# Kernel tuning notes

Hardware: AMD Instinct MI355X
Metric: run time of the kernel (lower is better)

Reference implementation:

```python
import jax, jax.numpy as jnp
import numpy as np

DM = 768            # d_model
DI = 1536           # d_inner = expand * d_model
P = 64              # headdim
H = DI // P         # 24 heads
N = 64              # d_state (Mamba2Simple default)
K = 4               # d_conv
CONVD = DI + 2 * N  # 1664
D_IN_PROJ = 2 * DI + 2 * N + H  # 3224
BATCH = 2
NVAL = 1024
L = NVAL
EPS = 1e-5

# static tail_order / swap_order index (transpose the rows x cols token grid, reversed)
_rows = int(NVAL ** 0.5)
_t = np.arange(NVAL).reshape(_rows, -1).T
_t = NVAL - 1 - _t
TAIL = _t.reshape(-1)
SEQ = jnp.asarray(np.concatenate([np.arange(L - NVAL), TAIL + (L - NVAL)]))


def _make_params(key, prefix):
    ks = jax.random.split(key, 6)
    dt = jnp.exp(jax.random.uniform(ks[2], (H,), minval=np.log(1e-3), maxval=np.log(1e-1)))
    return {
        prefix + 'ln_w': jnp.ones(DM, jnp.float32),
        prefix + 'ln_b': jnp.zeros(DM, jnp.float32),
        prefix + 'in_w': jax.random.normal(ks[0], (D_IN_PROJ, DM), jnp.float32) * 0.02,
        prefix + 'conv_w': jax.random.normal(ks[1], (CONVD, K), jnp.float32) * 0.1,
        prefix + 'conv_b': jnp.zeros(CONVD, jnp.float32),
        prefix + 'dt_bias': jnp.log(jnp.expm1(dt)),  # inverse softplus of dt in [1e-3, 1e-1]
        prefix + 'A_log': jnp.log(jax.random.uniform(ks[3], (H,), minval=1.0, maxval=16.0)),
        prefix + 'D': jnp.ones(H, jnp.float32),
        prefix + 'norm_w': jnp.ones(DI, jnp.float32),
        prefix + 'out_w': jax.random.normal(ks[4], (DM, DI), jnp.float32) * 0.02,
    }


def setup_inputs() -> dict:
    key = jax.random.key(0)
    k1, k2, k3 = jax.random.split(key, 3)
    inp = {'x': jax.random.normal(k1, (BATCH, L, DM), dtype=jnp.float32)}
    inp.update(_make_params(k2, 'f_'))
    inp.update(_make_params(k3, 'b_'))
    return inp


def _layernorm(x, w, b):
    m = jnp.mean(x, -1, keepdims=True)
    v = jnp.mean((x - m) ** 2, -1, keepdims=True)
    return (x - m) * jax.lax.rsqrt(v + EPS) * w + b


def _mamba2(x, in_w, conv_w, conv_b, dt_bias, A_log, Dp, norm_w, out_w):
    Bsz, Lseq, _ = x.shape
    zxbcdt = x @ in_w.T                                   # [B,L,3224]
    z, xBC, dt = jnp.split(zxbcdt, [DI, DI + CONVD], axis=-1)
    dt = jax.nn.softplus(dt + dt_bias)                    # [B,L,H]
    # causal depthwise conv1d over channels
    xc = jnp.transpose(xBC, (0, 2, 1))                    # [B,C,L]
    xc = jax.lax.conv_general_dilated(xc, conv_w[:, None, :], (1,), [(K - 1, 0)],
                                      feature_group_count=CONVD)
    xBC = jax.nn.silu(jnp.transpose(xc, (0, 2, 1)) + conv_b)
    xs, Bm, Cm = jnp.split(xBC, [DI, DI + N], axis=-1)
    xs = xs.reshape(Bsz, Lseq, H, P)
    A = -jnp.exp(A_log)                                   # [H], negative

    def step(S, inp):
        dt_t, x_t, B_t, C_t = inp                         # [B,H],[B,H,P],[B,N],[B,N]
        dA = jnp.exp(dt_t * A)                            # [B,H]
        S = S * dA[..., None, None] + dt_t[..., None, None] * B_t[:, None, :, None] * x_t[:, :, None, :]
        y = jnp.einsum('bn,bhnp->bhp', C_t, S)
        return S, y

    S0 = jnp.zeros((Bsz, H, N, P), x.dtype)
    ins = (jnp.moveaxis(dt, 1, 0), jnp.moveaxis(xs, 1, 0),
           jnp.moveaxis(Bm, 1, 0), jnp.moveaxis(Cm, 1, 0))
    _, ys = jax.lax.scan(step, S0, ins)
    y = jnp.moveaxis(ys, 0, 1) + Dp[None, None, :, None] * xs  # D skip, [B,L,H,P]
    y = y.reshape(Bsz, Lseq, DI)
    # RMSNormGated: gate then rmsnorm
    y = y * jax.nn.silu(z)
    y = y * jax.lax.rsqrt(jnp.mean(y * y, -1, keepdims=True) + EPS) * norm_w
    return y @ out_w.T


def _wrap(x, ln_w, ln_b, *mp):
    return x + _mamba2(_layernorm(x, ln_w, ln_b), *mp)


def reference(x,
              f_ln_w, f_ln_b, f_in_w, f_conv_w, f_conv_b, f_dt_bias, f_A_log, f_D, f_norm_w, f_out_w,
              b_ln_w, b_ln_b, b_in_w, b_conv_w, b_conv_b, b_dt_bias, b_A_log, b_D, b_norm_w, b_out_w):
    left_right = _wrap(x, f_ln_w, f_ln_b, f_in_w, f_conv_w, f_conv_b, f_dt_bias, f_A_log, f_D, f_norm_w, f_out_w)
    xs = x[:, SEQ]
    down_up = _wrap(xs, b_ln_w, b_ln_b, b_in_w, b_conv_w, b_conv_b, b_dt_bias, b_A_log, b_D, b_norm_w, b_out_w)
    down_up = down_up[:, SEQ]
    return left_right + down_up
```

## Files before the change

### kernel.cpp

```cpp
#include <hip/hip_runtime.h>
#include <cstdint>

#define DM    768
#define DI    1536
#define PP    64
#define HH    24
#define NN    64
#define CONVD 1664
#define DINP  3224
#define NP1   3328
#define LL    1024
#define ROWS  2048
#define EPSF  1e-5f
#define NCHUNK 16
#define CLEN   64
#define CSTRIPE 208

typedef unsigned short ushortT;
typedef __attribute__((ext_vector_type(8))) __bf16 bf16x8;
typedef __attribute__((ext_vector_type(8))) unsigned short ushort8;
typedef __attribute__((ext_vector_type(4))) unsigned short ushort4v;
typedef __attribute__((ext_vector_type(4))) float f32x4;

__device__ __forceinline__ int seqmap(int t) { return 1023 - 32 * (t & 31) - (t >> 5); }

__device__ __forceinline__ ushortT f2bf(float f) {
  union { float f; unsigned u; } v; v.f = f;
  unsigned r = v.u + 0x7FFF + ((v.u >> 16) & 1);
  return (ushortT)(r >> 16);
}
__device__ __forceinline__ float bf2f(ushortT b) {
  union { unsigned u; float f; } v; v.u = ((unsigned)b) << 16;
  return v.f;
}

__device__ __forceinline__ void gload_lds16(const void* g, void* l) {
  __builtin_amdgcn_global_load_lds((const __attribute__((address_space(1))) void*)g,
                                   (__attribute__((address_space(3))) void*)l, 16, 0, 0);
}

#define SWZ(r, c) ((r) * 64 + ((c) ^ (((r) & 7) << 3)))
#define SWZ64(r, c) ((r) * 64 + ((c) ^ (((r) & 7) << 3)))

__global__ __launch_bounds__(256) void prep_kernel(const float* __restrict__ x,
    const float* __restrict__ wf, const float* __restrict__ bf_,
    const float* __restrict__ wb, const float* __restrict__ bb,
    ushortT* __restrict__ xln,
    const float* __restrict__ fw1, const float* __restrict__ bw1,
    const float* __restrict__ fw2, const float* __restrict__ bw2,
    ushortT* __restrict__ WP1, ushortT* __restrict__ W2) {
  __shared__ float lds[4];
  int bid = blockIdx.x;
  int tid = threadIdx.x;
  if (bid < 2048) {
    int b = bid >> 10, sr = bid & 1023;
    const float* xr = x + (size_t)bid * DM;
    float v0 = xr[tid], v1 = xr[tid + 256], v2 = xr[tid + 512];
    float s = v0 + v1 + v2;
    #pragma unroll
    for (int o = 32; o; o >>= 1) s += __shfl_xor(s, o, 64);
    if ((tid & 63) == 0) lds[tid >> 6] = s;
    __syncthreads();
    float mean = (lds[0] + lds[1] + lds[2] + lds[3]) * (1.f / 768.f);
    __syncthreads();
    float d0 = v0 - mean, d1 = v1 - mean, d2 = v2 - mean;
    float q = d0 * d0 + d1 * d1 + d2 * d2;
    #pragma unroll
    for (int o = 32; o; o >>= 1) q += __shfl_xor(q, o, 64);
    if ((tid & 63) == 0) lds[tid >> 6] = q;
    __syncthreads();
    float var = (lds[0] + lds[1] + lds[2] + lds[3]) * (1.f / 768.f);
    float rs = rsqrtf(var + EPSF);
    int t1 = seqmap(sr);
    ushortT* o0 = xln + (size_t)bid * DM;
    ushortT* o1 = xln + (size_t)(2048 + b * 1024 + t1) * DM;
    o0[tid]       = f2bf(d0 * rs * wf[tid]       + bf_[tid]);
    o0[tid + 256] = f2bf(d1 * rs * wf[tid + 256] + bf_[tid + 256]);
    o0[tid + 512] = f2bf(d2 * rs * wf[tid + 512] + bf_[tid + 512]);
    o1[tid]       = f2bf(d0 * rs * wb[tid]       + bb[tid]);
    o1[tid + 256] = f2bf(d1 * rs * wb[tid + 256] + bb[tid + 256]);
    o1[tid + 512] = f2bf(d2 * rs * wb[tid + 512] + bb[tid + 512]);
  } else {
    const long NW1 = (long)NP1 * DM, SW1 = (long)DINP * DM, NW2 = (long)DM * DI;
    const long tot8 = (2 * NW1 + 2 * NW2) >> 3;
    long nb = (long)gridDim.x - 2048;
    for (long i8 = (long)(bid - 2048) * 256 + tid; i8 < tot8; i8 += nb * 256) {
      long i = i8 << 3;
      const float* src = nullptr;
      ushortT* dst;
      if (i < NW1) {
        if (i < SW1) src = fw1 + i;
        dst = WP1 + i;
      } else if (i < 2 * NW1) {
        long j = i - NW1;
        if (j < SW1) src = bw1 + j;
        dst = WP1 + i;
      } else if (i < 2 * NW1 + NW2) {
        long j = i - 2 * NW1;
        src = fw2 + j;
        dst = W2 + j;
      } else {
        long j = i - 2 * NW1 - NW2;
        src = bw2 + j;
        dst = W2 + NW2 + j;
      }
      ushort8 o = {};
      if (src) {
        float4 a = *(const float4*)src;
        float4 b2 = *(const float4*)(src + 4);
        o[0] = f2bf(a.x);  o[1] = f2bf(a.y);  o[2] = f2bf(a.z);  o[3] = f2bf(a.w);
        o[4] = f2bf(b2.x); o[5] = f2bf(b2.y); o[6] = f2bf(b2.z); o[7] = f2bf(b2.w);
      }
      *(ushort8*)dst = o;
    }
  }
}

template<int MODE>
__global__ __launch_bounds__(256) void gemm_bf16(
    const ushortT* __restrict__ Aall, const ushortT* __restrict__ Ball,
    float* __restrict__ Cfall, ushortT* __restrict__ Cball,
    int K, int lda, int ldb, int ldc, long sA, long sB, long sCf, long sCb) {
  __shared__ ushortT sA2[2][128 * 64];
  __shared__ ushortT sB2[2][128 * 64];
  int gx = gridDim.x, gy = gridDim.y;
  int nwg = gx * gy * gridDim.z;
  int lid = blockIdx.x + gx * (blockIdx.y + gy * blockIdx.z);
  int cpx = nwg >> 3;
  int swz = (lid & 7) * cpx + (lid >> 3);
  int bx = swz % gx;
  int rest = swz / gx;
  int by = rest % gy, bz = rest / gy;
  const ushortT* A = Aall + (size_t)bz * sA;
  const ushortT* B = Ball + (size_t)bz * sB;
  int tid = threadIdx.x, lane = tid & 63, w = tid >> 6;
  int wm = w >> 1, wn = w & 1;
  int m0 = by * 128, n0 = bx * 128;
  int rA8 = lane >> 3;
  int cSw = ((lane & 7) << 3) ^ (((lane >> 3) & 7) << 3);
  f32x4 acc[4][4] = {};
  const int NT = K >> 6;
  int fr = lane & 15, kq = lane >> 4;

  auto STAGE = [&](int bf, int kt) {
    int kc = kt * 64 + cSw;
    #pragma unroll
    for (int c2 = 0; c2 < 4; ++c2) {
      int q = w * 4 + c2;
      gload_lds16(A + (size_t)(m0 + q * 8 + rA8) * lda + kc, &sA2[bf][q * 512]);
    }
    #pragma unroll
    for (int c2 = 0; c2 < 4; ++c2) {
      int q = w * 4 + c2;
      gload_lds16(B + (size_t)(n0 + q * 8 + rA8) * ldb + kc, &sB2[bf][q * 512]);
    }
  };

  STAGE(0, 0);
  int cur = 0;
  for (int kt = 0; kt < NT; ++kt) {
    if (kt + 1 < NT) {
      STAGE(cur ^ 1, kt + 1);
      asm volatile("s_waitcnt vmcnt(8)" ::: "memory");
    } else {
      asm volatile("s_waitcnt vmcnt(0)" ::: "memory");
    }
    __builtin_amdgcn_s_barrier();
    __builtin_amdgcn_sched_barrier(0);
    #pragma unroll
    for (int ks = 0; ks < 2; ++ks) {
      int kb = ks * 32 + kq * 8;
      bf16x8 af[4], bfr[4];
      #pragma unroll
      for (int i = 0; i < 4; ++i)
        af[i] = *(const bf16x8*)&sA2[cur][SWZ64(wm * 64 + i * 16 + fr, kb)];
      #pragma unroll
      for (int j = 0; j < 4; ++j)
        bfr[j] = *(const bf16x8*)&sB2[cur][SWZ64(wn * 64 + j * 16 + fr, kb)];
      #pragma unroll
      for (int i = 0; i < 4; ++i)
        #pragma unroll
        for (int j = 0; j < 4; ++j)
          acc[i][j] = __builtin_amdgcn_mfma_f32_16x16x32_bf16(af[i], bfr[j], acc[i][j], 0, 0, 0);
    }
    asm volatile("s_waitcnt lgkmcnt(0)" ::: "memory");
    __builtin_amdgcn_sched_barrier(0);
    __builtin_amdgcn_s_barrier();
    cur ^= 1;
  }
  int cr = (lane >> 4) * 4, cc = lane & 15;
  if (MODE == 1 && n0 >= 3200) {
    float* Cf = Cfall + (size_t)bz * sCf;
    #pragma unroll
    for (int i = 0; i < 4; ++i)
      #pragma unroll
      for (int j = 0; j < 4; ++j) {
        float* Cp = Cf + (size_t)(m0 + wm * 64 + i * 16 + cr) * 128 + (wn * 64 + j * 16 + cc);
        #pragma unroll
        for (int r = 0; r < 4; ++r) Cp[(size_t)r * 128] = acc[i][j][r];
      }
  } else {
    ushortT* Cb = Cball + (size_t)bz * sCb;
    #pragma unroll
    for (int i = 0; i < 4; ++i)
      #pragma unroll
      for (int j = 0; j < 4; ++j) {
        ushortT* Cp = Cb + (size_t)(m0 + wm * 64 + i * 16 + cr) * ldc + (n0 + wn * 64 + j * 16 + cc);
        #pragma unroll
        for (int r = 0; r < 4; ++r) Cp[(size_t)r * ldc] = f2bf(acc[i][j][r]);
      }
  }
}

__global__ __launch_bounds__(256) void conv_dt_kernel(const ushortT* __restrict__ zxb,
    const float* __restrict__ dtt,
    const float* __restrict__ cwf, const float* __restrict__ cbf,
    const float* __restrict__ cwb, const float* __restrict__ cbb,
    const float* __restrict__ dtbf, const float* __restrict__ alogf,
    const float* __restrict__ dtbb, const float* __restrict__ alogb,
    ushortT* __restrict__ xcb, float* __restrict__ dts, float* __restrict__ lda_) {
  __shared__ ushortT sZ[67][CSTRIPE];
  int stripe = blockIdx.x, chunk = blockIdx.y, dirb = blockIdx.z;
  int dir = dirb >> 1;
  int t0 = chunk * 64;
  size_t rowb = (size_t)dirb * 1024;
  const float* cw = dir ? cwb : cwf;
  const float* cb = dir ? cbb : cbf;
  int tid = threadIdx.x;
  int cbase = stripe * CSTRIPE;
  for (int idx = tid; idx < 67 * 26; idx += 256) {
    int r = idx / 26, u = idx % 26;
    int t = t0 - 3 + r;
    ushort8 v = {};
    if (t >= 0)
      v = *(const ushort8*)&zxb[(rowb + t) * NP1 + 1536 + cbase + u * 8];
    *(ushort8*)&sZ[r][u * 8] = v;
  }
  if (stripe == 0) {
    const float* dtb  = dir ? dtbb : dtbf;
    const float* alog = dir ? alogb : alogf;
    for (int i = tid; i < 64 * HH; i += 256) {
      int tt = i / HH, h = i % HH;
      size_t row = rowb + t0 + tt;
      float raw = dtt[row * 128 + h] + dtb[h];
      float dtv = raw > 20.f ? raw : log1pf(expf(raw));
      dts[row * HH + h] = dtv;
      lda_[row * HH + h] = -expf(alog[h]) * dtv;
    }
  }
  __syncthreads();
  for (int idx = tid; idx < 64 * 26; idx += 256) {
    int r = idx / 26, u = idx % 26;
    int c0 = cbase + u * 8;
    ushort8 x0 = *(const ushort8*)&sZ[r][u * 8];
    ushort8 x1 = *(const ushort8*)&sZ[r + 1][u * 8];
    ushort8 x2 = *(const ushort8*)&sZ[r + 2][u * 8];
    ushort8 x3 = *(const ushort8*)&sZ[r + 3][u * 8];
    ushort8 o;
    #pragma unroll
    for (int e = 0; e < 8; ++e) {
      int c = c0 + e;
      float acc = cb[c] + bf2f(x0[e]) * cw[c * 4 + 0] + bf2f(x1[e]) * cw[c * 4 + 1]
                + bf2f(x2[e]) * cw[c * 4 + 2] + bf2f(x3[e]) * cw[c * 4 + 3];
      o[e] = f2bf(acc / (1.f + expf(-acc)));
    }
    *(ushort8*)&xcb[(rowb + t0 + r) * CONVD + c0] = o;
  }
}

__global__ __launch_bounds__(256) void ssd_chunk_kernel(const ushortT* __restrict__ xcb,
    const float* __restrict__ dts, const float* __restrict__ lda_,
    ushortT* __restrict__ yb, ushortT* __restrict__ slocb, float* __restrict__ cwg,
    ushortT* __restrict__ cbg) {
  __shared__ ushortT sCb[4096];
  __shared__ ushortT sBb[4096];
  __shared__ ushortT sBT[4096];
  __shared__ ushortT sXT[4096];
  __shared__ ushortT sMb[4096];
  __shared__ float clog[64];
  __shared__ float dt64[64];
  __shared__ float wv64[64];
  int gh = blockIdx.x;
  int c  = blockIdx.y;
  int dir = gh / 48;
  int rem = gh % 48;
  int b = rem / 24, h = rem % 24;
  int tid = threadIdx.x, lane = tid & 63;
  int w = tid >> 6;
  size_t rowbase = ((size_t)dir * 2 + b) * 1024;
  size_t trow = rowbase + (size_t)c * CLEN;

  #pragma unroll
  for (int it2 = 0; it2 < 2; ++it2) {
    int idx2 = it2 * 256 + tid;
    int r = idx2 >> 3, c8 = (idx2 & 7) << 3;
    const ushortT* xrow = xcb + (trow + r) * CONVD;
    *(ushort8*)&sCb[SWZ(r, c8)] = *(const ushort8*)&xrow[1600 + c8];
    *(ushort8*)&sBb[SWZ(r, c8)] = *(const ushort8*)&xrow[1536 + c8];
  }
  {
    int p = lane;
    #pragma unroll
    for (int q = 0; q < 4; ++q) {
      int t4 = w * 16 + q * 4;
      ushortT a0 = xcb[(trow + t4 + 0) * CONVD + h * 64 + p];
      ushortT a1 = xcb[(trow + t4 + 1) * CONVD + h * 64 + p];
      ushortT a2 = xcb[(trow + t4 + 2) * CONVD + h * 64 + p];
      ushortT a3 = xcb[(trow + t4 + 3) * CONVD + h * 64 + p];
      int cT = t4 ^ ((p & 7) << 3);
      ushort4v v4 = {a0, a1, a2, a3};
      *(ushort4v*)&sXT[p * 64 + cT] = v4;
    }
  }
  if (tid < 64) {
    float ld = lda_[(trow + tid) * HH + h];
    float dtv = dts[(trow + tid) * HH + h];
    float v = ld;
    #pragma unroll
    for (int o = 1; o < 64; o <<= 1) {
      float u = __shfl_up(v, o, 64);
      if (tid >= o) v += u;
    }
    float tot = __shfl(v, 63, 64);
    clog[tid] = v;
    dt64[tid] = dtv;
    wv64[tid] = dtv * __expf(tot - v);
    cwg[(trow + tid) * HH + h] = __expf(v);
  }
  __syncthreads();

  if (h == 0) {
    ushortT* dst = cbg + ((size_t)((dir * 2 + b) * NCHUNK + c)) * 4096;
    for (int idx = tid; idx < 4096; idx += 256) dst[idx] = sCb[idx];
  }

  int fr = lane & 15, kq = lane >> 4;

  {
    int n = lane;
    #pragma unroll
    for (int q = 0; q < 4; ++q) {
      int s4 = w * 16 + q * 4;
      float b0 = bf2f(sBb[SWZ(s4 + 0, n)]) * wv64[s4 + 0];
      float b1 = bf2f(sBb[SWZ(s4 + 1, n)]) * wv64[s4 + 1];
      float b2 = bf2f(sBb[SWZ(s4 + 2, n)]) * wv64[s4 + 2];
      float b3 = bf2f(sBb[SWZ(s4 + 3, n)]) * wv64[s4 + 3];
      int cT = s4 ^ ((n & 7) << 3);
      ushort4v v4 = {f2bf(b0), f2bf(b1), f2bf(b2), f2bf(b3)};
      *(ushort4v*)&sBT[n * 64 + cT] = v4;
    }
  }
  f32x4 accG[4] = {};
  #pragma unroll
  for (int kt = 0; kt < 2; ++kt) {
    int kk = kt * 32 + kq * 8;
    bf16x8 af = *(const bf16x8*)&sCb[SWZ(w * 16 + fr, kk)];
    #pragma unroll
    for (int j = 0; j < 4; ++j) {
      bf16x8 bf_ = *(const bf16x8*)&sBb[SWZ(j * 16 + fr, kk)];
      accG[j] = __builtin_amdgcn_mfma_f32_16x16x32_bf16(af, bf_, accG[j], 0, 0, 0);
    }
  }
  #pragma unroll
  for (int j = 0; j < 4; ++j) {
    int s = j * 16 + fr;
    float cls = clog[s], dtv = dt64[s];
    #pragma unroll
    for (int r = 0; r < 4; ++r) {
      int t = w * 16 + kq * 4 + r;
      float dec = (s <= t) ? __expf(clog[t] - cls) * dtv : 0.f;
      sMb[SWZ(t, s)] = f2bf(accG[j][r] * dec);
    }
  }
  __syncthreads();

  f32x4 accY[4] = {}, accS[4] = {};
  #pragma unroll
  for (int kt = 0; kt < 2; ++kt) {
    int kk = kt * 32 + kq * 8;
    bf16x8 aM = *(const bf16x8*)&sMb[SWZ(w * 16 + fr, kk)];
    bf16x8 aB = *(const bf16x8*)&sBT[SWZ(w * 16 + fr, kk)];
    #pragma unroll
    for (int j = 0; j < 4; ++j) {
      bf16x8 bx = *(const bf16x8*)&sXT[SWZ(j * 16 + fr, kk)];
      accY[j] = __builtin_amdgcn_mfma_f32_16x16x32_bf16(aM, bx, accY[j], 0, 0, 0);
      accS[j] = __builtin_amdgcn_mfma_f32_16x16x32_bf16(aB, bx, accS[j], 0, 0, 0);
    }
  }
  ushortT* spb = slocb + ((size_t)gh * NCHUNK + c) * 4096;
  #pragma unroll
  for (int j = 0; j < 4; ++j) {
    #pragma unroll
    for (int r = 0; r < 4; ++r) {
      int t = w * 16 + kq * 4 + r;
      int p = j * 16 + fr;
      yb[(trow + t) * DI + h * 64 + p] = f2bf(accY[j][r]);
      spb[t * 64 + p] = f2bf(accS[j][r]);
    }
  }
}

__global__ __launch_bounds__(256) void chunk_prefix_kernel(
    const ushortT* __restrict__ slocb, const float* __restrict__ cwg,
    ushortT* __restrict__ sinitb) {
  __shared__ float ldsT[64 * 65];
  int gh = blockIdx.x;
  int dir = gh / 48;
  int rem = gh % 48;
  int b = rem / 24, h = rem % 24;
  int tid = threadIdx.x;
  size_t rowbase = ((size_t)dir * 2 + b) * 1024;
  float R[16];
  #pragma unroll
  for (int j = 0; j < 16; ++j) R[j] = 0.f;
  for (int c = 1; c < NCHUNK; ++c) {
    float W = cwg[(rowbase + (size_t)c * CLEN - 1) * HH + h];
    const ushortT* slot = slocb + ((size_t)gh * NCHUNK + (c - 1)) * 4096;
    #pragma unroll
    for (int j = 0; j < 16; ++j) {
      int idx = j * 256 + tid, n = idx >> 6, p = idx & 63;
      R[j] = __builtin_fmaf(R[j], W, bf2f(slot[idx]));
      ldsT[n * 65 + p] = R[j];
    }
    __syncthreads();
    ushortT* outp = sinitb + ((size_t)gh * (NCHUNK - 1) + (c - 1)) * 4096;
    #pragma unroll
    for (int j = 0; j < 16; ++j) {
      int idx = j * 256 + tid, p = idx >> 6, n = idx & 63;
      outp[SWZ(p, n)] = f2bf(ldsT[n * 65 + p]);
    }
    __syncthreads();
  }
}

__global__ __launch_bounds__(256) void fixup_kernel(
    const ushortT* __restrict__ cbg, const ushortT* __restrict__ sinitb,
    const float* __restrict__ cwg, ushortT* __restrict__ yib) {
  __shared__ ushortT sCb[4096];
  __shared__ ushortT sST[4096];
  int gh = blockIdx.x;
  int c = blockIdx.y + 1;
  int dir = gh / 48;
  int rem = gh % 48;
  int b = rem / 24, h = rem % 24;
  int tid = threadIdx.x, lane = tid & 63, w = tid >> 6;
  size_t rowbase = ((size_t)dir * 2 + b) * 1024;
  size_t trow = rowbase + (size_t)c * CLEN;
  const ushortT* cbSrc = cbg + ((size_t)((dir * 2 + b) * NCHUNK + c)) * 4096;
  const ushortT* stSrc = sinitb + ((size_t)gh * (NCHUNK - 1) + (c - 1)) * 4096;
  #pragma unroll
  for (int ph = 0; ph < 2; ++ph) {
    int base = ph * 2048 + w * 512;
    gload_lds16(cbSrc + base + lane * 8, &sCb[base]);
    gload_lds16(stSrc + base + lane * 8, &sST[base]);
  }
  __syncthreads();
  int fr = lane & 15, kq = lane >> 4;
  f32x4 accY[4] = {};
  #pragma unroll
  for (int kt = 0; kt < 2; ++kt) {
    int kk = kt * 32 + kq * 8;
    bf16x8 aC = *(const bf16x8*)&sCb[SWZ(w * 16 + fr, kk)];
    #pragma unroll
    for (int j = 0; j < 4; ++j) {
      bf16x8 bS = *(const bf16x8*)&sST[SWZ(j * 16 + fr, kk)];
      accY[j] = __builtin_amdgcn_mfma_f32_16x16x32_bf16(aC, bS, accY[j], 0, 0, 0);
    }
  }
  float cwv[4];
  #pragma unroll
  for (int r = 0; r < 4; ++r)
    cwv[r] = cwg[(trow + w * 16 + kq * 4 + r) * HH + h];
  #pragma unroll
  for (int j = 0; j < 4; ++j)
    #pragma unroll
    for (int r = 0; r < 4; ++r) {
      int t = w * 16 + kq * 4 + r, p = j * 16 + fr;
      yib[(trow + t) * DI + h * 64 + p] = f2bf(accY[j][r] * cwv[r]);
    }
}

__global__ __launch_bounds__(192) void gate_norm_kernel(
    const ushortT* __restrict__ yb, const ushortT* __restrict__ yib,
    const ushortT* __restrict__ zxb, const ushortT* __restrict__ xcb,
    const float* __restrict__ Df, const float* __restrict__ Db,
    const float* __restrict__ nwf, const float* __restrict__ nwb,
    ushortT* __restrict__ yn) {
  __shared__ float lds[3];
  int bid = blockIdx.x;
  int dir = bid >> 11;
  int t = bid & 1023;
  const float* Dp = dir ? Db : Df;
  const float* nw = dir ? nwb : nwf;
  int tid = threadIdx.x;
  int c0 = tid * 8;
  float v[8];
  float ss = 0.f;
  {
    ushort8 yv8 = *(const ushort8*)&yb[(size_t)bid * DI + c0];
    ushort8 zv8 = *(const ushort8*)&zxb[(size_t)bid * NP1 + c0];
    ushort8 xv8 = *(const ushort8*)&xcb[(size_t)bid * CONVD + c0];
    ushort8 yi8 = {};
    bool hasI = (t >= CLEN);
    if (hasI) yi8 = *(const ushort8*)&yib[(size_t)bid * DI + c0];
    float Dv = Dp[c0 >> 6];
    #pragma unroll
    for (int e = 0; e < 8; ++e) {
      float yv = bf2f(yv8[e]) + (hasI ? bf2f(yi8[e]) : 0.f) + Dv * bf2f(xv8[e]);
      float zv = bf2f(zv8[e]);
      yv *= zv / (1.f + expf(-zv));
      v[e] = yv;
      ss += yv * yv;
    }
  }
  #pragma unroll
  for (int o = 32; o; o >>= 1) ss += __shfl_xor(ss, o, 64);
  if ((tid & 63) == 0) lds[tid >> 6] = ss;
  __syncthreads();
  float ms = (lds[0] + lds[1] + lds[2]) * (1.f / 1536.f);
  float sc = rsqrtf(ms + EPSF);
  {
    ushort8 o8;
    #pragma unroll
    for (int e = 0; e < 8; ++e) o8[e] = f2bf(v[e] * sc * nw[c0 + e]);
    *(ushort8*)&yn[(size_t)bid * DI + c0] = o8;
  }
}

__global__ __launch_bounds__(128) void combine_kernel(const float* __restrict__ x,
    const ushortT* __restrict__ mf, const ushortT* __restrict__ mb,
    float* __restrict__ out) {
  int bid = blockIdx.x;
  int b = bid >> 10, t = bid & 1023;
  int st = seqmap(t);
  int tid = threadIdx.x;
  if (tid >= 96) return;
  int c0 = tid * 8;
  ushort8 fv = *(const ushort8*)&mf[(size_t)bid * DM + c0];
  ushort8 bv = *(const ushort8*)&mb[(size_t)(b * 1024 + st) * DM + c0];
  const float4 x0 = *(const float4*)&x[(size_t)bid * DM + c0];
  const float4 x1 = *(const float4*)&x[(size_t)bid * DM + c0 + 4];
  float4 o0, o1;
  o0.x = 2.f * x0.x + bf2f(fv[0]) + bf2f(bv[0]);
  o0.y = 2.f * x0.y + bf2f(fv[1]) + bf2f(bv[1]);
  o0.z = 2.f * x0.z + bf2f(fv[2]) + bf2f(bv[2]);
  o0.w = 2.f * x0.w + bf2f(fv[3]) + bf2f(bv[3]);
  o1.x = 2.f * x1.x + bf2f(fv[4]) + bf2f(bv[4]);
  o1.y = 2.f * x1.y + bf2f(fv[5]) + bf2f(bv[5]);
  o1.z = 2.f * x1.z + bf2f(fv[6]) + bf2f(bv[6]);
  o1.w = 2.f * x1.w + bf2f(fv[7]) + bf2f(bv[7]);
  *(float4*)&out[(size_t)bid * DM + c0] = o0;
  *(float4*)&out[(size_t)bid * DM + c0 + 4] = o1;
}

extern "C" void kernel_launch(void* const* d_in, const int* in_sizes, int n_in,
                              void* d_out, int out_size, void* d_ws, size_t ws_size,
                              hipStream_t stream) {
  const float* x       = (const float*)d_in[0];
  const float* f_ln_w  = (const float*)d_in[1];
  const float* f_ln_b  = (const float*)d_in[2];
  const float* f_in_w  = (const float*)d_in[3];
  const float* f_cw    = (const float*)d_in[4];
  const float* f_cb    = (const float*)d_in[5];
  const float* f_dtb   = (const float*)d_in[6];
  const float* f_alog  = (const float*)d_in[7];
  const float* f_D     = (const float*)d_in[8];
  const float* f_nw    = (const float*)d_in[9];
  const float* f_ow    = (const float*)d_in[10];
  const float* b_ln_w  = (const float*)d_in[11];
  const float* b_ln_b  = (const float*)d_in[12];
  const float* b_in_w  = (const float*)d_in[13];
  const float* b_cw    = (const float*)d_in[14];
  const float* b_cb    = (const float*)d_in[15];
  const float* b_dtb   = (const float*)d_in[16];
  const float* b_alog  = (const float*)d_in[17];
  const float* b_D     = (const float*)d_in[18];
  const float* b_nw    = (const float*)d_in[19];
  const float* b_ow    = (const float*)d_in[20];

  char* ws = (char*)d_ws;
  size_t off = 0;
  auto carve = [&](size_t bytes) -> char* {
    off = (off + 255) & ~(size_t)255;
    char* p = ws + off;
    off += bytes;
    return p;
  };
  ushortT* XLN   = (ushortT*)carve((size_t)2 * ROWS * DM * 2);
  ushortT* WP1   = (ushortT*)carve((size_t)2 * NP1 * DM * 2);
  ushortT* W2    = (ushortT*)carve((size_t)2 * DM * DI * 2);
  ushortT* ZXB   = (ushortT*)carve((size_t)2 * ROWS * NP1 * 2);
  float*   DTT   = (float*)carve((size_t)2 * ROWS * 128 * 4);
  ushortT* XCB   = (ushortT*)carve((size_t)2 * ROWS * CONVD * 2);
  float*   DTS   = (float*)carve((size_t)2 * ROWS * HH * 4);
  float*   LDA   = (float*)carve((size_t)2 * ROWS * HH * 4);
  ushortT* YB    = (ushortT*)carve((size_t)2 * ROWS * DI * 2);
  ushortT* YIB   = (ushortT*)carve((size_t)2 * ROWS * DI * 2);
  ushortT* YN    = (ushortT*)carve((size_t)2 * ROWS * DI * 2);
  ushortT* MOUTB = (ushortT*)carve((size_t)2 * ROWS * DM * 2);
  ushortT* SLOCB = (ushortT*)carve((size_t)96 * NCHUNK * 4096 * 2);
  ushortT* SINIB = (ushortT*)carve((size_t)96 * (NCHUNK - 1) * 4096 * 2);
  ushortT* CBG   = (ushortT*)carve((size_t)4 * NCHUNK * 4096 * 2);
  float*   CWG   = (float*)carve((size_t)2 * ROWS * HH * 4);

  prep_kernel<<<4096, 256, 0, stream>>>(x, f_ln_w, f_ln_b, b_ln_w, b_ln_b, XLN,
                                        f_in_w, b_in_w, f_ow, b_ow, WP1, W2);

  gemm_bf16<1><<<dim3(NP1 / 128, ROWS / 128, 2), 256, 0, stream>>>(
      XLN, WP1, DTT, ZXB, DM, DM, DM, NP1,
      (long)ROWS * DM, (long)NP1 * DM, (long)ROWS * 128, (long)ROWS * NP1);

  conv_dt_kernel<<<dim3(8, 16, 4), 256, 0, stream>>>(ZXB, DTT, f_cw, f_cb, b_cw, b_cb,
                                                     f_dtb, f_alog, b_dtb, b_alog,
                                                     XCB, DTS, LDA);

  ssd_chunk_kernel<<<dim3(96, NCHUNK), 256, 0, stream>>>(XCB, DTS, LDA, YB, SLOCB, CWG, CBG);
  chunk_prefix_kernel<<<96, 256, 0, stream>>>(SLOCB, CWG, SINIB);
  fixup_kernel<<<dim3(96, NCHUNK - 1), 256, 0, stream>>>(CBG, SINIB, CWG, YIB);

  gate_norm_kernel<<<4096, 192, 0, stream>>>(YB, YIB, ZXB, XCB, f_D, b_D, f_nw, b_nw, YN);

  gemm_bf16<0><<<dim3(DM / 128, ROWS / 128, 2), 256, 0, stream>>>(
      YN, W2, nullptr, MOUTB, DI, DI, DI, DM,
      (long)ROWS * DI, (long)DM * DI, 0, (long)ROWS * DM);

  combine_kernel<<<2048, 128, 0, stream>>>(x, MOUTB, MOUTB + (size_t)ROWS * DM, (float*)d_out);
}
```

Before: 159.4 us.

## Fuse conv/dt into SSD chunk kernel and fold combine into GEMM epilogue atomics

The conv1d and softplus/dt computation moves into the SSD chunk kernel, so each block reads raw zxb rows with a 3-row halo and convolves its own B, C and x slices in LDS. This removes the separate conv_dt kernel and the DTS/LDA buffers, and stores only the x part of xcb. The combine kernel is removed: prep writes 2*x into the output, and the out-projection GEMM atomically adds fp32 results into it, applying the seqmap permutation for the backward direction. In exchange, each SSD block recomputes the B/C convolution for its chunk (24 heads redundantly), and the fp32 atomics add contention and make summation order nondeterministic.

```diff
diff --git a/kernel.cpp b/kernel.cpp
--- a/kernel.cpp
+++ b/kernel.cpp
@@ -6,15 +6,13 @@
 #define PP    64
 #define HH    24
 #define NN    64
-#define CONVD 1664
-#define DINP  3224
 #define NP1   3328
 #define LL    1024
 #define ROWS  2048
+#define DINP  3224
 #define EPSF  1e-5f
 #define NCHUNK 16
 #define CLEN   64
-#define CSTRIPE 208
 
 typedef unsigned short ushortT;
 typedef __attribute__((ext_vector_type(8))) __bf16 bf16x8;
@@ -45,7 +43,7 @@
 __global__ __launch_bounds__(256) void prep_kernel(const float* __restrict__ x,
     const float* __restrict__ wf, const float* __restrict__ bf_,
     const float* __restrict__ wb, const float* __restrict__ bb,
-    ushortT* __restrict__ xln,
+    ushortT* __restrict__ xln, float* __restrict__ out,
     const float* __restrict__ fw1, const float* __restrict__ bw1,
     const float* __restrict__ fw2, const float* __restrict__ bw2,
     ushortT* __restrict__ WP1, ushortT* __restrict__ W2) {
@@ -56,6 +54,8 @@
     int b = bid >> 10, sr = bid & 1023;
     const float* xr = x + (size_t)bid * DM;
     float v0 = xr[tid], v1 = xr[tid + 256], v2 = xr[tid + 512];
+    float* outp = out + (size_t)bid * DM;
+    outp[tid] = 2.f * v0; outp[tid + 256] = 2.f * v1; outp[tid + 512] = 2.f * v2;
     float s = v0 + v1 + v2;
     #pragma unroll
     for (int o = 32; o; o >>= 1) s += __shfl_xor(s, o, 64);
@@ -199,6 +199,20 @@
         #pragma unroll
         for (int r = 0; r < 4; ++r) Cp[(size_t)r * 128] = acc[i][j][r];
       }
+  } else if (MODE == 2) {
+    #pragma unroll
+    for (int i = 0; i < 4; ++i)
+      #pragma unroll
+      for (int r = 0; r < 4; ++r) {
+        int mrow = m0 + wm * 64 + i * 16 + cr + r;
+        int brow;
+        if (bz == 0) brow = mrow;
+        else { int bb2 = mrow >> 10, tt2 = mrow & 1023; brow = bb2 * 1024 + seqmap(tt2); }
+        float* orow = Cfall + (size_t)brow * DM;
+        #pragma unroll
+        for (int j = 0; j < 4; ++j)
+          atomicAdd(&orow[n0 + wn * 64 + j * 16 + cc], acc[i][j][r]);
+      }
   } else {
     ushortT* Cb = Cball + (size_t)bz * sCb;
     #pragma unroll
@@ -212,74 +226,27 @@
   }
 }
 
-__global__ __launch_bounds__(256) void conv_dt_kernel(const ushortT* __restrict__ zxb,
+__global__ __launch_bounds__(256) void ssd_chunk_kernel(const ushortT* __restrict__ zxb,
     const float* __restrict__ dtt,
     const float* __restrict__ cwf, const float* __restrict__ cbf,
     const float* __restrict__ cwb, const float* __restrict__ cbb,
     const float* __restrict__ dtbf, const float* __restrict__ alogf,
     const float* __restrict__ dtbb, const float* __restrict__ alogb,
-    ushortT* __restrict__ xcb, float* __restrict__ dts, float* __restrict__ lda_) {
-  __shared__ ushortT sZ[67][CSTRIPE];
-  int stripe = blockIdx.x, chunk = blockIdx.y, dirb = blockIdx.z;
-  int dir = dirb >> 1;
-  int t0 = chunk * 64;
-  size_t rowb = (size_t)dirb * 1024;
-  const float* cw = dir ? cwb : cwf;
-  const float* cb = dir ? cbb : cbf;
-  int tid = threadIdx.x;
-  int cbase = stripe * CSTRIPE;
-  for (int idx = tid; idx < 67 * 26; idx += 256) {
-    int r = idx / 26, u = idx % 26;
-    int t = t0 - 3 + r;
-    ushort8 v = {};
-    if (t >= 0)
-      v = *(const ushort8*)&zxb[(rowb + t) * NP1 + 1536 + cbase + u * 8];
-    *(ushort8*)&sZ[r][u * 8] = v;
-  }
-  if (stripe == 0) {
-    const float* dtb  = dir ? dtbb : dtbf;
-    const float* alog = dir ? alogb : alogf;
-    for (int i = tid; i < 64 * HH; i += 256) {
-      int tt = i / HH, h = i % HH;
-      size_t row = rowb + t0 + tt;
-      float raw = dtt[row * 128 + h] + dtb[h];
-      float dtv = raw > 20.f ? raw : log1pf(expf(raw));
-      dts[row * HH + h] = dtv;
-      lda_[row * HH + h] = -expf(alog[h]) * dtv;
-    }
-  }
-  __syncthreads();
-  for (int idx = tid; idx < 64 * 26; idx += 256) {
-    int r = idx / 26, u = idx % 26;
-    int c0 = cbase + u * 8;
-    ushort8 x0 = *(const ushort8*)&sZ[r][u * 8];
-    ushort8 x1 = *(const ushort8*)&sZ[r + 1][u * 8];
-    ushort8 x2 = *(const ushort8*)&sZ[r + 2][u * 8];
-    ushort8 x3 = *(const ushort8*)&sZ[r + 3][u * 8];
-    ushort8 o;
-    #pragma unroll
-    for (int e = 0; e < 8; ++e) {
-      int c = c0 + e;
-      float acc = cb[c] + bf2f(x0[e]) * cw[c * 4 + 0] + bf2f(x1[e]) * cw[c * 4 + 1]
-                + bf2f(x2[e]) * cw[c * 4 + 2] + bf2f(x3[e]) * cw[c * 4 + 3];
-      o[e] = f2bf(acc / (1.f + expf(-acc)));
-    }
-    *(ushort8*)&xcb[(rowb + t0 + r) * CONVD + c0] = o;
-  }
-}
-
-__global__ __launch_bounds__(256) void ssd_chunk_kernel(const ushortT* __restrict__ xcb,
-    const float* __restrict__ dts, const float* __restrict__ lda_,
+    ushortT* __restrict__ xcb,
     ushortT* __restrict__ yb, ushortT* __restrict__ slocb, float* __restrict__ cwg,
     ushortT* __restrict__ cbg) {
   __shared__ ushortT sCb[4096];
   __shared__ ushortT sBb[4096];
-  __shared__ ushortT sBT[4096];
   __shared__ ushortT sXT[4096];
-  __shared__ ushortT sMb[4096];
+  __shared__ ushortT sPool[12864];
   __shared__ float clog[64];
   __shared__ float dt64[64];
   __shared__ float wv64[64];
+  ushortT* sBT    = sPool;
+  ushortT* sMb    = sPool + 4096;
+  ushortT* sRawBC = sPool;
+  ushortT* sRawX  = sPool + 8576;
+
   int gh = blockIdx.x;
   int c  = blockIdx.y;
   int dir = gh / 48;
@@ -288,33 +255,31 @@
   int tid = threadIdx.x, lane = tid & 63;
   int w = tid >> 6;
   size_t rowbase = ((size_t)dir * 2 + b) * 1024;
-  size_t trow = rowbase + (size_t)c * CLEN;
-
-  #pragma unroll
-  for (int it2 = 0; it2 < 2; ++it2) {
-    int idx2 = it2 * 256 + tid;
-    int r = idx2 >> 3, c8 = (idx2 & 7) << 3;
-    const ushortT* xrow = xcb + (trow + r) * CONVD;
-    *(ushort8*)&sCb[SWZ(r, c8)] = *(const ushort8*)&xrow[1600 + c8];
-    *(ushort8*)&sBb[SWZ(r, c8)] = *(const ushort8*)&xrow[1536 + c8];
-  }
-  {
-    int p = lane;
-    #pragma unroll
-    for (int q = 0; q < 4; ++q) {
-      int t4 = w * 16 + q * 4;
-      ushortT a0 = xcb[(trow + t4 + 0) * CONVD + h * 64 + p];
-      ushortT a1 = xcb[(trow + t4 + 1) * CONVD + h * 64 + p];
-      ushortT a2 = xcb[(trow + t4 + 2) * CONVD + h * 64 + p];
-      ushortT a3 = xcb[(trow + t4 + 3) * CONVD + h * 64 + p];
-      int cT = t4 ^ ((p & 7) << 3);
-      ushort4v v4 = {a0, a1, a2, a3};
-      *(ushort4v*)&sXT[p * 64 + cT] = v4;
-    }
+  int t0 = c * CLEN;
+  size_t trow = rowbase + (size_t)t0;
+  const float* cw   = dir ? cwb : cwf;
+  const float* cb   = dir ? cbb : cbf;
+  const float* dtb  = dir ? dtbb : dtbf;
+  const float* alog = dir ? alogb : alogf;
+
+  for (int idx = tid; idx < 67 * 16; idx += 256) {
+    int r = idx >> 4, g = idx & 15;
+    int t = t0 - 3 + r;
+    ushort8 v = {};
+    if (t >= 0) v = *(const ushort8*)&zxb[(rowbase + t) * NP1 + 3072 + g * 8];
+    *(ushort8*)&sRawBC[r * 128 + g * 8] = v;
+  }
+  for (int idx = tid; idx < 67 * 8; idx += 256) {
+    int r = idx >> 3, g = idx & 7;
+    int t = t0 - 3 + r;
+    ushort8 v = {};
+    if (t >= 0) v = *(const ushort8*)&zxb[(rowbase + t) * NP1 + 1536 + h * 64 + g * 8];
+    *(ushort8*)&sRawX[r * 64 + g * 8] = v;
   }
   if (tid < 64) {
-    float ld = lda_[(trow + tid) * HH + h];
-    float dtv = dts[(trow + tid) * HH + h];
+    float raw = dtt[(trow + tid) * 128 + h] + dtb[h];
+    float dtv = raw > 20.f ? raw : log1pf(expf(raw));
+    float ld = -expf(alog[h]) * dtv;
     float v = ld;
     #pragma unroll
     for (int o = 1; o < 64; o <<= 1) {
@@ -326,6 +291,62 @@
     dt64[tid] = dtv;
     wv64[tid] = dtv * __expf(tot - v);
     cwg[(trow + tid) * HH + h] = __expf(v);
+  }
+  __syncthreads();
+
+  {
+    int g = tid & 15;
+    int r0 = tid >> 4;
+    int cc8 = g * 8;
+    float cbv[8], cwv[8][4];
+    #pragma unroll
+    for (int e = 0; e < 8; ++e) {
+      int gc = 1536 + cc8 + e;
+      cbv[e] = cb[gc];
+      #pragma unroll
+      for (int k = 0; k < 4; ++k) cwv[e][k] = cw[gc * 4 + k];
+    }
+    #pragma unroll
+    for (int rr = 0; rr < 4; ++rr) {
+      int r = r0 + rr * 16;
+      ushort8 x0 = *(const ushort8*)&sRawBC[(r + 0) * 128 + cc8];
+      ushort8 x1 = *(const ushort8*)&sRawBC[(r + 1) * 128 + cc8];
+      ushort8 x2 = *(const ushort8*)&sRawBC[(r + 2) * 128 + cc8];
+      ushort8 x3 = *(const ushort8*)&sRawBC[(r + 3) * 128 + cc8];
+      ushort8 o;
+      #pragma unroll
+      for (int e = 0; e < 8; ++e) {
+        float a = cbv[e] + bf2f(x0[e]) * cwv[e][0] + bf2f(x1[e]) * cwv[e][1]
+                + bf2f(x2[e]) * cwv[e][2] + bf2f(x3[e]) * cwv[e][3];
+        o[e] = f2bf(a / (1.f + expf(-a)));
+      }
+      if (cc8 < 64) *(ushort8*)&sBb[SWZ(r, cc8)] = o;
+      else          *(ushort8*)&sCb[SWZ(r, cc8 - 64)] = o;
+    }
+  }
+  {
+    int p = lane;
+    int ch = h * 64 + p;
+    float cbv = cb[ch];
+    float w0 = cw[ch * 4], w1 = cw[ch * 4 + 1], w2 = cw[ch * 4 + 2], w3 = cw[ch * 4 + 3];
+    #pragma unroll
+    for (int q = 0; q < 4; ++q) {
+      int t4 = w * 16 + q * 4;
+      float rv[7];
+      #pragma unroll
+      for (int rr = 0; rr < 7; ++rr) rv[rr] = bf2f(sRawX[(t4 + rr) * 64 + p]);
+      ushort4v v4;
+      #pragma unroll
+      for (int i = 0; i < 4; ++i) {
+        float a = cbv + rv[i] * w0 + rv[i + 1] * w1 + rv[i + 2] * w2 + rv[i + 3] * w3;
+        v4[i] = f2bf(a / (1.f + expf(-a)));
+      }
+      int cT = t4 ^ ((p & 7) << 3);
+      *(ushort4v*)&sXT[p * 64 + cT] = v4;
+      #pragma unroll
+      for (int i = 0; i < 4; ++i)
+        xcb[(trow + t4 + i) * 1536 + ch] = v4[i];
+    }
   }
   __syncthreads();
 
@@ -499,7 +520,7 @@
   {
     ushort8 yv8 = *(const ushort8*)&yb[(size_t)bid * DI + c0];
     ushort8 zv8 = *(const ushort8*)&zxb[(size_t)bid * NP1 + c0];
-    ushort8 xv8 = *(const ushort8*)&xcb[(size_t)bid * CONVD + c0];
+    ushort8 xv8 = *(const ushort8*)&xcb[(size_t)bid * 1536 + c0];
     ushort8 yi8 = {};
     bool hasI = (t >= CLEN);
     if (hasI) yi8 = *(const ushort8*)&yib[(size_t)bid * DI + c0];
@@ -525,32 +546,6 @@
     for (int e = 0; e < 8; ++e) o8[e] = f2bf(v[e] * sc * nw[c0 + e]);
     *(ushort8*)&yn[(size_t)bid * DI + c0] = o8;
   }
-}
-
-__global__ __launch_bounds__(128) void combine_kernel(const float* __restrict__ x,
-    const ushortT* __restrict__ mf, const ushortT* __restrict__ mb,
-    float* __restrict__ out) {
-  int bid = blockIdx.x;
-  int b = bid >> 10, t = bid & 1023;
-  int st = seqmap(t);
-  int tid = threadIdx.x;
-  if (tid >= 96) return;
-  int c0 = tid * 8;
-  ushort8 fv = *(const ushort8*)&mf[(size_t)bid * DM + c0];
-  ushort8 bv = *(const ushort8*)&mb[(size_t)(b * 1024 + st) * DM + c0];
-  const float4 x0 = *(const float4*)&x[(size_t)bid * DM + c0];
-  const float4 x1 = *(const float4*)&x[(size_t)bid * DM + c0 + 4];
-  float4 o0, o1;
-  o0.x = 2.f * x0.x + bf2f(fv[0]) + bf2f(bv[0]);
-  o0.y = 2.f * x0.y + bf2f(fv[1]) + bf2f(bv[1]);
-  o0.z = 2.f * x0.z + bf2f(fv[2]) + bf2f(bv[2]);
-  o0.w = 2.f * x0.w + bf2f(fv[3]) + bf2f(bv[3]);
-  o1.x = 2.f * x1.x + bf2f(fv[4]) + bf2f(bv[4]);
-  o1.y = 2.f * x1.y + bf2f(fv[5]) + bf2f(bv[5]);
-  o1.z = 2.f * x1.z + bf2f(fv[6]) + bf2f(bv[6]);
-  o1.w = 2.f * x1.w + bf2f(fv[7]) + bf2f(bv[7]);
-  *(float4*)&out[(size_t)bid * DM + c0] = o0;
-  *(float4*)&out[(size_t)bid * DM + c0 + 4] = o1;
 }
 
 extern "C" void kernel_launch(void* const* d_in, const int* in_sizes, int n_in,
@@ -577,6 +572,7 @@
   const float* b_D     = (const float*)d_in[18];
   const float* b_nw    = (const float*)d_in[19];
   const float* b_ow    = (const float*)d_in[20];
+  float* out = (float*)d_out;
 
   char* ws = (char*)d_ws;
   size_t off = 0;
@@ -591,38 +587,32 @@
   ushortT* W2    = (ushortT*)carve((size_t)2 * DM * DI * 2);
   ushortT* ZXB   = (ushortT*)carve((size_t)2 * ROWS * NP1 * 2);
   float*   DTT   = (float*)carve((size_t)2 * ROWS * 128 * 4);
-  ushortT* XCB   = (ushortT*)carve((size_t)2 * ROWS * CONVD * 2);
-  float*   DTS   = (float*)carve((size_t)2 * ROWS * HH * 4);
-  float*   LDA   = (float*)carve((size_t)2 * ROWS * HH * 4);
+  ushortT* XCB   = (ushortT*)carve((size_t)2 * ROWS * 1536 * 2);
   ushortT* YB    = (ushortT*)carve((size_t)2 * ROWS * DI * 2);
   ushortT* YIB   = (ushortT*)carve((size_t)2 * ROWS * DI * 2);
   ushortT* YN    = (ushortT*)carve((size_t)2 * ROWS * DI * 2);
-  ushortT* MOUTB = (ushortT*)carve((size_t)2 * ROWS * DM * 2);
   ushortT* SLOCB = (ushortT*)carve((size_t)96 * NCHUNK * 4096 * 2);
   ushortT* SINIB = (ushortT*)carve((size_t)96 * (NCHUNK - 1) * 4096 * 2);
   ushortT* CBG   = (ushortT*)carve((size_t)4 * NCHUNK * 4096 * 2);
   float*   CWG   = (float*)carve((size_t)2 * ROWS * HH * 4);
 
-  prep_kernel<<<4096, 256, 0, stream>>>(x, f_ln_w, f_ln_b, b_ln_w, b_ln_b, XLN,
+  prep_kernel<<<4096, 256, 0, stream>>>(x, f_ln_w, f_ln_b, b_ln_w, b_ln_b, XLN, out,
                                         f_in_w, b_in_w, f_ow, b_ow, WP1, W2);
 
   gemm_bf16<1><<<dim3(NP1 / 128, ROWS / 128, 2), 256, 0, stream>>>(
       XLN, WP1, DTT, ZXB, DM, DM, DM, NP1,
       (long)ROWS * DM, (long)NP1 * DM, (long)ROWS * 128, (long)ROWS * NP1);
 
-  conv_dt_kernel<<<dim3(8, 16, 4), 256, 0, stream>>>(ZXB, DTT, f_cw, f_cb, b_cw, b_cb,
-                                                     f_dtb, f_alog, b_dtb, b_alog,
-                                                     XCB, DTS, LDA);
-
-  ssd_chunk_kernel<<<dim3(96, NCHUNK), 256, 0, stream>>>(XCB, DTS, LDA, YB, SLOCB, CWG, CBG);
+  ssd_chunk_kernel<<<dim3(96, NCHUNK), 256, 0, stream>>>(
+      ZXB, DTT, f_cw, f_cb, b_cw, b_cb, f_dtb, f_alog, b_dtb, b_alog,
+      XCB, YB, SLOCB, CWG, CBG);
+
   chunk_prefix_kernel<<<96, 256, 0, stream>>>(SLOCB, CWG, SINIB);
   fixup_kernel<<<dim3(96, NCHUNK - 1), 256, 0, stream>>>(CBG, SINIB, CWG, YIB);
 
   gate_norm_kernel<<<4096, 192, 0, stream>>>(YB, YIB, ZXB, XCB, f_D, b_D, f_nw, b_nw, YN);
 
-  gemm_bf16<0><<<dim3(DM / 128, ROWS / 128, 2), 256, 0, stream>>>(
-      YN, W2, nullptr, MOUTB, DI, DI, DI, DM,
-      (long)ROWS * DI, (long)DM * DI, 0, (long)ROWS * DM);
-
-  combine_kernel<<<2048, 128, 0, stream>>>(x, MOUTB, MOUTB + (size_t)ROWS * DM, (float*)d_out);
-}
+  gemm_bf16<2><<<dim3(DM / 128, ROWS / 128, 2), 256, 0, stream>>>(
+      YN, W2, out, nullptr, DI, DI, DI, DM,
+      (long)ROWS * DI, (long)DM * DI, 0, 0);
+}
```

After: 156.0 us. 1.02x faster.
